# Kernel optimization log

Measured on AMD Instinct MI355X. Metric: run time of the kernel, lower is better.

## Reference

```python
import jax, jax.numpy as jnp
import numpy as np

SOFTCAP = 50.0  # GEMMA2_TANH_SCALE
N_HEADS = 16

def _rope(x, cos, sin):
    # x: [B,S,H,D]; cos/sin: [S,D/2]; interleaved complex pairs as in apply_rotary_emb
    x0 = x[..., 0::2]
    x1 = x[..., 1::2]
    c = cos[None, :, None, :]
    s = sin[None, :, None, :]
    r0 = x0 * c - x1 * s
    r1 = x0 * s + x1 * c
    return jnp.stack([r0, r1], axis=-1).reshape(x.shape)

def setup_inputs() -> dict:
    key = jax.random.key(0)
    ks = jax.random.split(key, 5)
    B, S, DM = 1, 2048, 2048
    hd = DM // N_HEADS
    scale = 1.0 / np.sqrt(DM)
    x = jax.random.normal(ks[0], (B, S, DM), jnp.float32)
    wq = jax.random.normal(ks[1], (DM, DM), jnp.float32) * scale
    wk = jax.random.normal(ks[2], (DM, DM), jnp.float32) * scale
    wv = jax.random.normal(ks[3], (DM, DM), jnp.float32) * scale
    wo = jax.random.normal(ks[4], (DM, DM), jnp.float32) * scale
    # rotary tables, theta=10000 as in llama
    inv_freq = 10000.0 ** (-jnp.arange(0, hd, 2, dtype=jnp.float32) / hd)
    ang = jnp.arange(S, dtype=jnp.float32)[:, None] * inv_freq[None, :]
    return {"x": x, "wq": wq, "wk": wk, "wv": wv, "wo": wo,
            "freqs_cos": jnp.cos(ang), "freqs_sin": jnp.sin(ang)}

def reference(x, wq, wk, wv, wo, freqs_cos, freqs_sin):
    B, S, DM = x.shape
    H = N_HEADS
    hd = DM // H
    q = (x @ wq).reshape(B, S, H, hd)
    k = (x @ wk).reshape(B, S, H, hd)
    v = (x @ wv).reshape(B, S, H, hd)
    q = _rope(q, freqs_cos, freqs_sin)
    k = _rope(k, freqs_cos, freqs_sin)
    # scores [B,H,S,S]
    scores = jnp.einsum('bqhd,bkhd->bhqk', q, k) / jnp.sqrt(jnp.float32(hd))
    scores = SOFTCAP * jnp.tanh(scores / SOFTCAP)  # gemma2 tanh soft-cap
    causal = jnp.tril(jnp.ones((S, S), dtype=bool))
    scores = jnp.where(causal[None, None], scores, -jnp.inf)
    p = jax.nn.softmax(scores, axis=-1)
    o = jnp.einsum('bhqk,bkhd->bqhd', p, v).reshape(B, S, DM)
    return o @ wo
```

## Files before the change

### kernel.cpp

```cpp
#include <hip/hip_runtime.h>
#include <hip/hip_bf16.h>

typedef __attribute__((ext_vector_type(8))) short short8;
typedef __attribute__((ext_vector_type(4))) short short4v;
typedef __attribute__((ext_vector_type(4))) float f32x4;
typedef __attribute__((ext_vector_type(4))) float float4v;

#define S_LEN 2048
#define DMODEL 2048
#define N_HEADS 16
#define HEAD_DIM 128

__device__ __forceinline__ float bf2f(__hip_bfloat16 b) { return __bfloat162float(b); }
__device__ __forceinline__ __hip_bfloat16 f2bf(float f) { return __float2bfloat16(f); }
__device__ __forceinline__ short bfs(float f) {
    union { __hip_bfloat16 b; short s; } x; x.b = __float2bfloat16(f); return x.s;
}
__device__ __forceinline__ float sbf(short s) {
    union { short s; __hip_bfloat16 b; } x; x.s = s; return __bfloat162float(x.b);
}

#if __has_builtin(__builtin_amdgcn_global_load_lds)
#define HAVE_ASYNC_LDS 1
#else
#define HAVE_ASYNC_LDS 0
#endif

__device__ __forceinline__ void stage16(const __hip_bfloat16* g, __hip_bfloat16* ldsbase, int lane) {
#if HAVE_ASYNC_LDS
    __builtin_amdgcn_global_load_lds(
        (const __attribute__((address_space(1))) unsigned int*)g,
        (__attribute__((address_space(3))) unsigned int*)ldsbase,
        16, 0, 0);
#else
    *(short8*)((char*)ldsbase + lane * 16) = *(const short8*)g;
#endif
}

__global__ __launch_bounds__(256) void prep(const float* __restrict__ x,
                                            const float* __restrict__ w0,
                                            const float* __restrict__ w1,
                                            const float* __restrict__ w2,
                                            const float* __restrict__ w3,
                                            __hip_bfloat16* __restrict__ xb,
                                            __hip_bfloat16* __restrict__ o0,
                                            __hip_bfloat16* __restrict__ o1,
                                            __hip_bfloat16* __restrict__ o2,
                                            __hip_bfloat16* __restrict__ o3) {
    const int z = blockIdx.z;
    if (z == 4) {
        size_t base = ((size_t)(blockIdx.y * 64 + blockIdx.x) * 256 + (threadIdx.y * 32 + threadIdx.x)) * 4;
        float4v v = *(const float4v*)(x + base);
        short4v p;
        p.x = bfs(v.x); p.y = bfs(v.y); p.z = bfs(v.z); p.w = bfs(v.w);
        *(short4v*)(xb + base) = p;
        return;
    }
    const float* in = (z == 0) ? w0 : (z == 1) ? w1 : (z == 2) ? w2 : w3;
    __hip_bfloat16* out = (z == 0) ? o0 : (z == 1) ? o1 : (z == 2) ? o2 : o3;
    __shared__ __hip_bfloat16 tile[32][33];
    int bx = blockIdx.x * 32;
    int by = blockIdx.y * 32;
    int tx = threadIdx.x;
    int ty = threadIdx.y;
    for (int i = ty; i < 32; i += 8)
        tile[i][tx] = f2bf(in[(size_t)(by + i) * DMODEL + bx + tx]);
    __syncthreads();
    for (int i = ty; i < 32; i += 8)
        out[(size_t)(bx + i) * DMODEL + by + tx] = tile[tx][i];
}

__global__ __launch_bounds__(256) void gemm_qkv(const __hip_bfloat16* __restrict__ A,
                                                const __hip_bfloat16* __restrict__ Bq,
                                                const __hip_bfloat16* __restrict__ Bk,
                                                const __hip_bfloat16* __restrict__ Bv,
                                                __hip_bfloat16* __restrict__ Cq,
                                                __hip_bfloat16* __restrict__ Ck,
                                                __hip_bfloat16* __restrict__ Cvt,
                                                const float* __restrict__ fc,
                                                const float* __restrict__ fs) {
    __shared__ alignas(16) __hip_bfloat16 As[2][128 * 32];
    __shared__ alignas(16) __hip_bfloat16 Bs[2][128 * 32];
    const int which = blockIdx.x >> 4;
    const __hip_bfloat16* Bt = (which == 0) ? Bq : (which == 1) ? Bk : Bv;
    const int tid = threadIdx.x;
    const int wave = tid >> 6;
    const int lane = tid & 63;
    const int lane15 = lane & 15;
    const int quad = lane >> 4;
    const int m0 = blockIdx.y * 128;
    const int n0 = (blockIdx.x & 15) * 128;
    const int wm = (wave >> 1) * 64;
    const int wn = (wave & 1) * 64;

    f32x4 acc[4][4];
    for (int i = 0; i < 4; ++i)
        for (int j = 0; j < 4; ++j)
            acc[i][j] = {0.f, 0.f, 0.f, 0.f};

    const int rA = lane >> 2;
    const int cA = (lane & 3) * 8;

    for (int k0 = 0; k0 < DMODEL; k0 += 64) {
        __syncthreads();
        for (int h = 0; h < 2; ++h) {
            int kk = k0 + h * 32;
            for (int c = 0; c < 4; ++c) {
                int chunk = wave * 4 + c;
                if (chunk < 8) {
                    int r = chunk * 16 + rA;
                    stage16(A + (size_t)(m0 + r) * DMODEL + kk + cA, As[h] + chunk * 512, lane);
                } else {
                    int r = (chunk - 8) * 16 + rA;
                    stage16(Bt + (size_t)(n0 + r) * DMODEL + kk + cA, Bs[h] + (chunk - 8) * 512, lane);
                }
            }
        }
#if HAVE_ASYNC_LDS
        asm volatile("s_waitcnt vmcnt(0)" ::: "memory");
#endif
        __syncthreads();

        for (int h = 0; h < 2; ++h) {
            short8 af[4], bfr[4];
            for (int mt = 0; mt < 4; ++mt)
                af[mt] = *(const short8*)(As[h] + (wm + mt * 16 + lane15) * 32 + quad * 8);
            for (int nt = 0; nt < 4; ++nt)
                bfr[nt] = *(const short8*)(Bs[h] + (wn + nt * 16 + lane15) * 32 + quad * 8);
            for (int mt = 0; mt < 4; ++mt)
                for (int nt = 0; nt < 4; ++nt)
                    acc[mt][nt] = __builtin_amdgcn_mfma_f32_16x16x32_bf16(af[mt], bfr[nt], acc[mt][nt], 0, 0, 0);
        }
    }

    if (which < 2) {
        __hip_bfloat16* C = (which == 0) ? Cq : Ck;
        for (int mt = 0; mt < 4; ++mt)
            for (int nt = 0; nt < 4; ++nt) {
                int col = n0 + wn + nt * 16 + lane15;
                int j = (col & 127) >> 1;
                bool odd = col & 1;
                for (int i = 0; i < 4; ++i) {
                    int row = m0 + wm + mt * 16 + quad * 4 + i;
                    float v = acc[mt][nt][i];
                    float p = __shfl_xor(v, 1, 64);
                    float c = fc[row * 64 + j];
                    float sn = fs[row * 64 + j];
                    float r = odd ? (p * sn + v * c) : (v * c - p * sn);
                    C[(size_t)row * DMODEL + col] = f2bf(r);
                }
            }
    } else {
        for (int mt = 0; mt < 4; ++mt) {
            int rowbase = m0 + wm + mt * 16 + quad * 4;
            for (int nt = 0; nt < 4; ++nt) {
                int col = n0 + wn + nt * 16 + lane15;
                short4v pk;
                pk.x = bfs(acc[mt][nt][0]);
                pk.y = bfs(acc[mt][nt][1]);
                pk.z = bfs(acc[mt][nt][2]);
                pk.w = bfs(acc[mt][nt][3]);
                *(short4v*)(Cvt + (size_t)col * S_LEN + rowbase) = pk;
            }
        }
    }
}

__global__ __launch_bounds__(256) void gemm_out(const __hip_bfloat16* __restrict__ A,
                                                const __hip_bfloat16* __restrict__ Bt,
                                                float* __restrict__ C) {
    __shared__ alignas(16) __hip_bfloat16 As[2][128 * 32];
    __shared__ alignas(16) __hip_bfloat16 Bs[2][64 * 32];
    const int tid = threadIdx.x;
    const int wave = tid >> 6;
    const int lane = tid & 63;
    const int lane15 = lane & 15;
    const int quad = lane >> 4;
    const int m0 = blockIdx.y * 128;
    const int n0 = blockIdx.x * 64;
    const int wm = (wave >> 1) * 64;
    const int wn = (wave & 1) * 32;

    f32x4 acc[4][2];
    for (int i = 0; i < 4; ++i)
        for (int j = 0; j < 2; ++j)
            acc[i][j] = {0.f, 0.f, 0.f, 0.f};

    const int rA = lane >> 2;
    const int cA = (lane & 3) * 8;

    for (int k0 = 0; k0 < DMODEL; k0 += 64) {
        __syncthreads();
        for (int h = 0; h < 2; ++h) {
            int kk = k0 + h * 32;
            for (int c = 0; c < 3; ++c) {
                int chunk = wave * 3 + c;
                if (chunk < 8) {
                    int r = chunk * 16 + rA;
                    stage16(A + (size_t)(m0 + r) * DMODEL + kk + cA, As[h] + chunk * 512, lane);
                } else {
                    int r = (chunk - 8) * 16 + rA;
                    stage16(Bt + (size_t)(n0 + r) * DMODEL + kk + cA, Bs[h] + (chunk - 8) * 512, lane);
                }
            }
        }
#if HAVE_ASYNC_LDS
        asm volatile("s_waitcnt vmcnt(0)" ::: "memory");
#endif
        __syncthreads();

        for (int h = 0; h < 2; ++h) {
            short8 af[4], bfr[2];
            for (int mt = 0; mt < 4; ++mt)
                af[mt] = *(const short8*)(As[h] + (wm + mt * 16 + lane15) * 32 + quad * 8);
            for (int nt = 0; nt < 2; ++nt)
                bfr[nt] = *(const short8*)(Bs[h] + (wn + nt * 16 + lane15) * 32 + quad * 8);
            for (int mt = 0; mt < 4; ++mt)
                for (int nt = 0; nt < 2; ++nt)
                    acc[mt][nt] = __builtin_amdgcn_mfma_f32_16x16x32_bf16(af[mt], bfr[nt], acc[mt][nt], 0, 0, 0);
        }
    }

    for (int mt = 0; mt < 4; ++mt)
        for (int nt = 0; nt < 2; ++nt)
            for (int i = 0; i < 4; ++i) {
                int row = m0 + wm + mt * 16 + quad * 4 + i;
                int col = n0 + wn + nt * 16 + lane15;
                C[(size_t)row * DMODEL + col] = acc[mt][nt][i];
            }
}

__global__ __launch_bounds__(256) void flash_attn(const __hip_bfloat16* __restrict__ Q,
                                                  const __hip_bfloat16* __restrict__ Kb,
                                                  const __hip_bfloat16* __restrict__ Vt,
                                                  __hip_bfloat16* __restrict__ O) {
    __shared__ alignas(16) short Ks[32][136];
    __shared__ alignas(16) short Vs[128][40];
    __shared__ alignas(16) short Pl[4][16][40];
    const int tid = threadIdx.x;
    const int wave = tid >> 6;
    const int lane = tid & 63;
    const int lane15 = lane & 15;
    const int quad = lane >> 4;
    const int bx = blockIdx.x;
    const int u = bx & 255;
    const int head = u & 15;
    const int qp = u >> 4;
    const int qb = (bx < 256) ? (31 - qp) : qp;
    const int qbase = qb * 64;
    const int q0w = qbase + wave * 16;
    const int nkt = 2 * qb + 2;
    const float K1 = 0.08838834764831845f * (1.0f / 25.0f);

    const __hip_bfloat16* Qh = Q + (size_t)q0w * DMODEL + head * HEAD_DIM;
    short8 qf[4];
    for (int kk = 0; kk < 4; ++kk)
        qf[kk] = *(const short8*)(Qh + (size_t)lane15 * DMODEL + kk * 32 + quad * 8);

    f32x4 acc[8];
    for (int i = 0; i < 8; ++i) acc[i] = {0.f, 0.f, 0.f, 0.f};
    float lpart[4] = {0.f, 0.f, 0.f, 0.f};

    const int krow = tid >> 3, kcol = (tid & 7) * 16;
    const int vrow = tid >> 1, vcol = (tid & 1) * 16;
    const __hip_bfloat16* Kg = Kb + (size_t)krow * DMODEL + head * HEAD_DIM + kcol;
    const __hip_bfloat16* Vg = Vt + (size_t)(head * HEAD_DIM + vrow) * S_LEN + vcol;

    short8 gk0 = *(const short8*)(Kg);
    short8 gk1 = *(const short8*)(Kg + 8);
    short8 gv0 = *(const short8*)(Vg);
    short8 gv1 = *(const short8*)(Vg + 8);

    for (int kt = 0; kt < nkt; ++kt) {
        const int kb = kt * 32;
        __syncthreads();
        *(short8*)&Ks[krow][kcol] = gk0;
        *(short8*)&Ks[krow][kcol + 8] = gk1;
        *(short8*)&Vs[vrow][vcol] = gv0;
        *(short8*)&Vs[vrow][vcol + 8] = gv1;
        __syncthreads();

        if (kt + 1 < nkt) {
            const __hip_bfloat16* Kg2 = Kg + (size_t)(kb + 32) * DMODEL;
            const __hip_bfloat16* Vg2 = Vg + kb + 32;
            gk0 = *(const short8*)(Kg2);
            gk1 = *(const short8*)(Kg2 + 8);
            gv0 = *(const short8*)(Vg2);
            gv1 = *(const short8*)(Vg2 + 8);
        }

        if (kb <= q0w + 15) {
            f32x4 sc[2];
            sc[0] = {0.f, 0.f, 0.f, 0.f};
            sc[1] = {0.f, 0.f, 0.f, 0.f};
            for (int c = 0; c < 2; ++c)
                for (int kk = 0; kk < 4; ++kk) {
                    short8 kf = *(const short8*)&Ks[c * 16 + lane15][kk * 32 + quad * 8];
                    sc[c] = __builtin_amdgcn_mfma_f32_16x16x32_bf16(qf[kk], kf, sc[c], 0, 0, 0);
                }

            const bool masked = (kb + 31 > q0w);
            const int key0 = kb + lane15;
            const int key1 = kb + 16 + lane15;
            for (int i = 0; i < 4; ++i) {
                float e0 = __expf(sc[0][i] * K1);
                float e1 = __expf(sc[1][i] * K1);
                float c0 = __builtin_fmaf(-100.0f, __builtin_amdgcn_rcpf(e0 + 1.0f), 40.0f);
                float c1 = __builtin_fmaf(-100.0f, __builtin_amdgcn_rcpf(e1 + 1.0f), 40.0f);
                float p0 = __expf(c0);
                float p1 = __expf(c1);
                if (masked) {
                    int q = q0w + quad * 4 + i;
                    if (key0 > q) p0 = 0.f;
                    if (key1 > q) p1 = 0.f;
                }
                short b0 = bfs(p0), b1 = bfs(p1);
                lpart[i] += sbf(b0) + sbf(b1);
                Pl[wave][quad * 4 + i][lane15] = b0;
                Pl[wave][quad * 4 + i][16 + lane15] = b1;
            }
            asm volatile("s_waitcnt lgkmcnt(0)" ::: "memory");
            short8 pf = *(const short8*)&Pl[wave][lane15][quad * 8];
            asm volatile("" ::: "memory");
            for (int nt = 0; nt < 8; ++nt) {
                short8 vf = *(const short8*)&Vs[nt * 16 + lane15][quad * 8];
                acc[nt] = __builtin_amdgcn_mfma_f32_16x16x32_bf16(pf, vf, acc[nt], 0, 0, 0);
            }
        }
    }

    for (int i = 0; i < 4; ++i) {
        float l = lpart[i];
        l += __shfl_xor(l, 1, 64);
        l += __shfl_xor(l, 2, 64);
        l += __shfl_xor(l, 4, 64);
        l += __shfl_xor(l, 8, 64);
        float inv = 1.0f / l;
        int row = q0w + quad * 4 + i;
        for (int nt = 0; nt < 8; ++nt) {
            int col = head * HEAD_DIM + nt * 16 + lane15;
            O[(size_t)row * DMODEL + col] = f2bf(acc[nt][i] * inv);
        }
    }
}

extern "C" void kernel_launch(void* const* d_in, const int* in_sizes, int n_in,
                              void* d_out, int out_size, void* d_ws, size_t ws_size,
                              hipStream_t stream) {
    const float* x  = (const float*)d_in[0];
    const float* wq = (const float*)d_in[1];
    const float* wk = (const float*)d_in[2];
    const float* wv = (const float*)d_in[3];
    const float* wo = (const float*)d_in[4];
    const float* fc = (const float*)d_in[5];
    const float* fs = (const float*)d_in[6];
    float* out = (float*)d_out;

    char* ws = (char*)d_ws;
    const size_t MB8 = (size_t)2048 * 2048 * sizeof(__hip_bfloat16);
    __hip_bfloat16* wq_t = (__hip_bfloat16*)(ws + 0 * MB8);
    __hip_bfloat16* wk_t = (__hip_bfloat16*)(ws + 1 * MB8);
    __hip_bfloat16* wv_t = (__hip_bfloat16*)(ws + 2 * MB8);
    __hip_bfloat16* wo_t = (__hip_bfloat16*)(ws + 3 * MB8);
    __hip_bfloat16* Qb   = (__hip_bfloat16*)(ws + 4 * MB8);
    __hip_bfloat16* Kbuf = (__hip_bfloat16*)(ws + 5 * MB8);
    __hip_bfloat16* Vt   = (__hip_bfloat16*)(ws + 6 * MB8);
    __hip_bfloat16* attn = wq_t;
    __hip_bfloat16* x_bf = (__hip_bfloat16*)d_out;

    prep<<<dim3(64, 64, 5), dim3(32, 8), 0, stream>>>(x, wq, wk, wv, wo,
                                                      x_bf, wq_t, wk_t, wv_t, wo_t);

    gemm_qkv<<<dim3(48, 16), 256, 0, stream>>>(x_bf, wq_t, wk_t, wv_t, Qb, Kbuf, Vt, fc, fs);

    flash_attn<<<512, 256, 0, stream>>>(Qb, Kbuf, Vt, attn);

    gemm_out<<<dim3(32, 16), 256, 0, stream>>>(attn, wo_t, out);
}
```

Baseline: 321.6 us.

## Split-K QKV GEMM with separate reduce+RoPE pass and wider transpose tiles

Splits the QKV projection GEMM into two K-halves, doubling the block count from 768 to 1536 for better CU occupancy. A new reduce_rope kernel sums the two bf16 partials and applies RoPE. The prep kernel now uses 64x64 tiles with vectorized loads and stores. The cost is extra memory traffic for the partial buffers, an extra kernel launch, and some accuracy loss because the partials are rounded to bf16 before the sum.

```diff
diff --git a/kernel.cpp b/kernel.cpp
--- a/kernel.cpp
+++ b/kernel.cpp
@@ -48,37 +48,171 @@
                                             __hip_bfloat16* __restrict__ o2,
                                             __hip_bfloat16* __restrict__ o3) {
     const int z = blockIdx.z;
+    const int tid = threadIdx.x;
     if (z == 4) {
-        size_t base = ((size_t)(blockIdx.y * 64 + blockIdx.x) * 256 + (threadIdx.y * 32 + threadIdx.x)) * 4;
-        float4v v = *(const float4v*)(x + base);
+        size_t base = (((size_t)blockIdx.y * 32 + blockIdx.x) * 256 + tid) * 16;
+        for (int i = 0; i < 4; ++i) {
+            float4v v = *(const float4v*)(x + base + i * 4);
+            short4v p;
+            p.x = bfs(v.x); p.y = bfs(v.y); p.z = bfs(v.z); p.w = bfs(v.w);
+            *(short4v*)((short*)xb + base + i * 4) = p;
+        }
+        return;
+    }
+    const float* in = (z == 0) ? w0 : (z == 1) ? w1 : (z == 2) ? w2 : w3;
+    __hip_bfloat16* out = (z == 0) ? o0 : (z == 1) ? o1 : (z == 2) ? o2 : o3;
+    __shared__ short tile[64][68];
+    const int bx = blockIdx.x * 64;
+    const int by = blockIdx.y * 64;
+    const int c4 = (tid & 15) * 4;
+    for (int rr = 0; rr < 4; ++rr) {
+        int r = (tid >> 4) + rr * 16;
+        float4v v = *(const float4v*)(in + (size_t)(by + r) * DMODEL + bx + c4);
         short4v p;
         p.x = bfs(v.x); p.y = bfs(v.y); p.z = bfs(v.z); p.w = bfs(v.w);
-        *(short4v*)(xb + base) = p;
-        return;
-    }
-    const float* in = (z == 0) ? w0 : (z == 1) ? w1 : (z == 2) ? w2 : w3;
-    __hip_bfloat16* out = (z == 0) ? o0 : (z == 1) ? o1 : (z == 2) ? o2 : o3;
-    __shared__ __hip_bfloat16 tile[32][33];
-    int bx = blockIdx.x * 32;
-    int by = blockIdx.y * 32;
-    int tx = threadIdx.x;
-    int ty = threadIdx.y;
-    for (int i = ty; i < 32; i += 8)
-        tile[i][tx] = f2bf(in[(size_t)(by + i) * DMODEL + bx + tx]);
+        *(short4v*)&tile[r][c4] = p;
+    }
     __syncthreads();
-    for (int i = ty; i < 32; i += 8)
-        out[(size_t)(bx + i) * DMODEL + by + tx] = tile[tx][i];
-}
-
-__global__ __launch_bounds__(256) void gemm_qkv(const __hip_bfloat16* __restrict__ A,
-                                                const __hip_bfloat16* __restrict__ Bq,
-                                                const __hip_bfloat16* __restrict__ Bk,
-                                                const __hip_bfloat16* __restrict__ Bv,
-                                                __hip_bfloat16* __restrict__ Cq,
-                                                __hip_bfloat16* __restrict__ Ck,
-                                                __hip_bfloat16* __restrict__ Cvt,
-                                                const float* __restrict__ fc,
-                                                const float* __restrict__ fs) {
+    const int oc = tid >> 2;
+    const int s0 = (tid & 3) * 16;
+    short8 a, b;
+    for (int i = 0; i < 8; ++i) ((short*)&a)[i] = tile[s0 + i][oc];
+    for (int i = 0; i < 8; ++i) ((short*)&b)[i] = tile[s0 + 8 + i][oc];
+    *(short8*)((short*)out + (size_t)(bx + oc) * DMODEL + by + s0) = a;
+    *(short8*)((short*)out + (size_t)(bx + oc) * DMODEL + by + s0 + 8) = b;
+}
+
+__global__ __launch_bounds__(256) void gemm_qkv_sk(const __hip_bfloat16* __restrict__ A,
+                                                   const __hip_bfloat16* __restrict__ Bq,
+                                                   const __hip_bfloat16* __restrict__ Bk,
+                                                   const __hip_bfloat16* __restrict__ Bv,
+                                                   __hip_bfloat16* __restrict__ Q0,
+                                                   __hip_bfloat16* __restrict__ Q1,
+                                                   __hip_bfloat16* __restrict__ K0,
+                                                   __hip_bfloat16* __restrict__ K1,
+                                                   __hip_bfloat16* __restrict__ V0t,
+                                                   __hip_bfloat16* __restrict__ V1t) {
+    __shared__ alignas(16) __hip_bfloat16 As[128 * 32];
+    __shared__ alignas(16) __hip_bfloat16 Bs[128 * 32];
+    const int bx = blockIdx.x;
+    const int which = bx >> 5;
+    const int kh = (bx >> 4) & 1;
+    const __hip_bfloat16* Bt = (which == 0) ? Bq : (which == 1) ? Bk : Bv;
+    const int tid = threadIdx.x;
+    const int wave = tid >> 6;
+    const int lane = tid & 63;
+    const int lane15 = lane & 15;
+    const int quad = lane >> 4;
+    const int m0 = blockIdx.y * 128;
+    const int n0 = (bx & 15) * 128;
+    const int wm = (wave >> 1) * 64;
+    const int wn = (wave & 1) * 64;
+
+    f32x4 acc[4][4];
+    for (int i = 0; i < 4; ++i)
+        for (int j = 0; j < 4; ++j)
+            acc[i][j] = {0.f, 0.f, 0.f, 0.f};
+
+    const int rA = lane >> 2;
+    const int cA = (lane & 3) * 8;
+    const int kbeg = kh * 1024;
+
+    for (int k0 = kbeg; k0 < kbeg + 1024; k0 += 32) {
+        __syncthreads();
+        for (int c = 0; c < 4; ++c) {
+            int chunk = wave * 4 + c;
+            if (chunk < 8) {
+                int r = chunk * 16 + rA;
+                stage16(A + (size_t)(m0 + r) * DMODEL + k0 + cA, As + chunk * 512, lane);
+            } else {
+                int r = (chunk - 8) * 16 + rA;
+                stage16(Bt + (size_t)(n0 + r) * DMODEL + k0 + cA, Bs + (chunk - 8) * 512, lane);
+            }
+        }
+#if HAVE_ASYNC_LDS
+        asm volatile("s_waitcnt vmcnt(0)" ::: "memory");
+#endif
+        __syncthreads();
+
+        short8 af[4], bfr[4];
+        for (int mt = 0; mt < 4; ++mt)
+            af[mt] = *(const short8*)(As + (wm + mt * 16 + lane15) * 32 + quad * 8);
+        for (int nt = 0; nt < 4; ++nt)
+            bfr[nt] = *(const short8*)(Bs + (wn + nt * 16 + lane15) * 32 + quad * 8);
+        for (int mt = 0; mt < 4; ++mt)
+            for (int nt = 0; nt < 4; ++nt)
+                acc[mt][nt] = __builtin_amdgcn_mfma_f32_16x16x32_bf16(af[mt], bfr[nt], acc[mt][nt], 0, 0, 0);
+    }
+
+    if (which < 2) {
+        __hip_bfloat16* C = (which == 0) ? (kh ? Q1 : Q0) : (kh ? K1 : K0);
+        for (int mt = 0; mt < 4; ++mt)
+            for (int nt = 0; nt < 4; ++nt)
+                for (int i = 0; i < 4; ++i) {
+                    int row = m0 + wm + mt * 16 + quad * 4 + i;
+                    int col = n0 + wn + nt * 16 + lane15;
+                    C[(size_t)row * DMODEL + col] = f2bf(acc[mt][nt][i]);
+                }
+    } else {
+        __hip_bfloat16* Vp = kh ? V1t : V0t;
+        for (int mt = 0; mt < 4; ++mt) {
+            int rowbase = m0 + wm + mt * 16 + quad * 4;
+            for (int nt = 0; nt < 4; ++nt) {
+                int col = n0 + wn + nt * 16 + lane15;
+                short4v pk;
+                pk.x = bfs(acc[mt][nt][0]);
+                pk.y = bfs(acc[mt][nt][1]);
+                pk.z = bfs(acc[mt][nt][2]);
+                pk.w = bfs(acc[mt][nt][3]);
+                *(short4v*)((short*)Vp + (size_t)col * S_LEN + rowbase) = pk;
+            }
+        }
+    }
+}
+
+__global__ __launch_bounds__(256) void reduce_rope(__hip_bfloat16* __restrict__ Q0,
+                                                   const __hip_bfloat16* __restrict__ Q1,
+                                                   __hip_bfloat16* __restrict__ K0,
+                                                   const __hip_bfloat16* __restrict__ K1,
+                                                   __hip_bfloat16* __restrict__ V0,
+                                                   const __hip_bfloat16* __restrict__ V1,
+                                                   const float* __restrict__ fc,
+                                                   const float* __restrict__ fs) {
+    const int z = blockIdx.z;
+    __hip_bfloat16* P0 = (z == 0) ? Q0 : (z == 1) ? K0 : V0;
+    const __hip_bfloat16* P1 = (z == 0) ? Q1 : (z == 1) ? K1 : V1;
+    size_t i0 = ((size_t)blockIdx.x * 256 + threadIdx.x) * 8;
+    short8 a = *(const short8*)((const short*)P0 + i0);
+    short8 b = *(const short8*)((const short*)P1 + i0);
+    float s[8];
+    for (int i = 0; i < 8; ++i) s[i] = sbf(((short*)&a)[i]) + sbf(((short*)&b)[i]);
+    short8 o;
+    if (z < 2) {
+        int row = (int)(i0 >> 11);
+        int col = (int)(i0 & 2047);
+        int j0 = (col & 127) >> 1;
+        for (int p = 0; p < 4; ++p) {
+            float c = fc[row * 64 + j0 + p];
+            float sn = fs[row * 64 + j0 + p];
+            float e = s[2 * p], od = s[2 * p + 1];
+            ((short*)&o)[2 * p]     = bfs(e * c - od * sn);
+            ((short*)&o)[2 * p + 1] = bfs(e * sn + od * c);
+        }
+    } else {
+        for (int i = 0; i < 8; ++i) ((short*)&o)[i] = bfs(s[i]);
+    }
+    *(short8*)((short*)P0 + i0) = o;
+}
+
+__global__ __launch_bounds__(256) void gemm_qkv_fused(const __hip_bfloat16* __restrict__ A,
+                                                      const __hip_bfloat16* __restrict__ Bq,
+                                                      const __hip_bfloat16* __restrict__ Bk,
+                                                      const __hip_bfloat16* __restrict__ Bv,
+                                                      __hip_bfloat16* __restrict__ Cq,
+                                                      __hip_bfloat16* __restrict__ Ck,
+                                                      __hip_bfloat16* __restrict__ Cvt,
+                                                      const float* __restrict__ fc,
+                                                      const float* __restrict__ fs) {
     __shared__ alignas(16) __hip_bfloat16 As[2][128 * 32];
     __shared__ alignas(16) __hip_bfloat16 Bs[2][128 * 32];
     const int which = blockIdx.x >> 4;
@@ -92,15 +226,12 @@
     const int n0 = (blockIdx.x & 15) * 128;
     const int wm = (wave >> 1) * 64;
     const int wn = (wave & 1) * 64;
-
     f32x4 acc[4][4];
     for (int i = 0; i < 4; ++i)
         for (int j = 0; j < 4; ++j)
             acc[i][j] = {0.f, 0.f, 0.f, 0.f};
-
     const int rA = lane >> 2;
     const int cA = (lane & 3) * 8;
-
     for (int k0 = 0; k0 < DMODEL; k0 += 64) {
         __syncthreads();
         for (int h = 0; h < 2; ++h) {
@@ -120,7 +251,6 @@
         asm volatile("s_waitcnt vmcnt(0)" ::: "memory");
 #endif
         __syncthreads();
-
         for (int h = 0; h < 2; ++h) {
             short8 af[4], bfr[4];
             for (int mt = 0; mt < 4; ++mt)
@@ -132,7 +262,6 @@
                     acc[mt][nt] = __builtin_amdgcn_mfma_f32_16x16x32_bf16(af[mt], bfr[nt], acc[mt][nt], 0, 0, 0);
         }
     }
-
     if (which < 2) {
         __hip_bfloat16* C = (which == 0) ? Cq : Ck;
         for (int mt = 0; mt < 4; ++mt)
@@ -160,7 +289,7 @@
                 pk.y = bfs(acc[mt][nt][1]);
                 pk.z = bfs(acc[mt][nt][2]);
                 pk.w = bfs(acc[mt][nt][3]);
-                *(short4v*)(Cvt + (size_t)col * S_LEN + rowbase) = pk;
+                *(short4v*)((short*)Cvt + (size_t)col * S_LEN + rowbase) = pk;
             }
         }
     }
@@ -180,15 +309,12 @@
     const int n0 = blockIdx.x * 64;
     const int wm = (wave >> 1) * 64;
     const int wn = (wave & 1) * 32;
-
     f32x4 acc[4][2];
     for (int i = 0; i < 4; ++i)
         for (int j = 0; j < 2; ++j)
             acc[i][j] = {0.f, 0.f, 0.f, 0.f};
-
     const int rA = lane >> 2;
     const int cA = (lane & 3) * 8;
-
     for (int k0 = 0; k0 < DMODEL; k0 += 64) {
         __syncthreads();
         for (int h = 0; h < 2; ++h) {
@@ -208,7 +334,6 @@
         asm volatile("s_waitcnt vmcnt(0)" ::: "memory");
 #endif
         __syncthreads();
-
         for (int h = 0; h < 2; ++h) {
             short8 af[4], bfr[2];
             for (int mt = 0; mt < 4; ++mt)
@@ -220,7 +345,6 @@
                     acc[mt][nt] = __builtin_amdgcn_mfma_f32_16x16x32_bf16(af[mt], bfr[nt], acc[mt][nt], 0, 0, 0);
         }
     }
-
     for (int mt = 0; mt < 4; ++mt)
         for (int nt = 0; nt < 2; ++nt)
             for (int i = 0; i < 4; ++i) {
@@ -362,18 +486,26 @@
     __hip_bfloat16* wk_t = (__hip_bfloat16*)(ws + 1 * MB8);
     __hip_bfloat16* wv_t = (__hip_bfloat16*)(ws + 2 * MB8);
     __hip_bfloat16* wo_t = (__hip_bfloat16*)(ws + 3 * MB8);
-    __hip_bfloat16* Qb   = (__hip_bfloat16*)(ws + 4 * MB8);
-    __hip_bfloat16* Kbuf = (__hip_bfloat16*)(ws + 5 * MB8);
-    __hip_bfloat16* Vt   = (__hip_bfloat16*)(ws + 6 * MB8);
-    __hip_bfloat16* attn = wq_t;
+    __hip_bfloat16* s4   = (__hip_bfloat16*)(ws + 4 * MB8);
+    __hip_bfloat16* s5   = (__hip_bfloat16*)(ws + 5 * MB8);
+    __hip_bfloat16* s6   = (__hip_bfloat16*)(ws + 6 * MB8);
+    __hip_bfloat16* s7   = (__hip_bfloat16*)(ws + 7 * MB8);
+    __hip_bfloat16* s8   = (__hip_bfloat16*)(ws + 8 * MB8);
+    __hip_bfloat16* s9   = (__hip_bfloat16*)(ws + 9 * MB8);
     __hip_bfloat16* x_bf = (__hip_bfloat16*)d_out;
 
-    prep<<<dim3(64, 64, 5), dim3(32, 8), 0, stream>>>(x, wq, wk, wv, wo,
-                                                      x_bf, wq_t, wk_t, wv_t, wo_t);
-
-    gemm_qkv<<<dim3(48, 16), 256, 0, stream>>>(x_bf, wq_t, wk_t, wv_t, Qb, Kbuf, Vt, fc, fs);
-
-    flash_attn<<<512, 256, 0, stream>>>(Qb, Kbuf, Vt, attn);
-
-    gemm_out<<<dim3(32, 16), 256, 0, stream>>>(attn, wo_t, out);
-}
+    prep<<<dim3(32, 32, 5), 256, 0, stream>>>(x, wq, wk, wv, wo, x_bf, wq_t, wk_t, wv_t, wo_t);
+
+    if (ws_size >= 10 * MB8) {
+        gemm_qkv_sk<<<dim3(96, 16), 256, 0, stream>>>(x_bf, wq_t, wk_t, wv_t,
+                                                      s4, s7, s5, s8, s6, s9);
+        reduce_rope<<<dim3(2048, 1, 3), 256, 0, stream>>>(s4, s7, s5, s8, s6, s9, fc, fs);
+        flash_attn<<<512, 256, 0, stream>>>(s4, s5, s6, wq_t);
+        gemm_out<<<dim3(32, 16), 256, 0, stream>>>(wq_t, wo_t, out);
+    } else {
+        gemm_qkv_fused<<<dim3(48, 16), 256, 0, stream>>>(x_bf, wq_t, wk_t, wv_t,
+                                                         s4, s5, s6, fc, fs);
+        flash_attn<<<512, 256, 0, stream>>>(s4, s5, s6, wq_t);
+        gemm_out<<<dim3(32, 16), 256, 0, stream>>>(wq_t, wo_t, out);
+    }
+}
```

New measurement: 307.9 us. 1.04x faster.
